# Optimization experiments

Measured on AMD Instinct MI355X. Metric: run time of the kernel, lower is better.

## Reference

```python
import jax, jax.numpy as jnp
import numpy as np

D_Q = 512
D_O = 256  # = d_v = d_k = d_o
N_HEAD = 8
BN_EPS = 1e-5
LEAK = 0.1


def setup_inputs() -> dict:
    key = jax.random.key(0)
    ks = jax.random.split(key, 8)
    s = 0.02
    inp = {
        "q": jax.random.normal(ks[0], (64, D_Q), dtype=jnp.float32),
        "v": jax.random.normal(ks[1], (64, D_O, 32, 32), dtype=jnp.float32),
        "w_q": jax.random.normal(ks[2], (D_O, D_Q), dtype=jnp.float32) * s,
        "b_q": jnp.zeros((D_O,), jnp.float32),
        "w_kc": jax.random.normal(ks[3], (D_O, D_O), dtype=jnp.float32) * s,
        "b_kc": jnp.zeros((D_O,), jnp.float32),
        "w_kd": jax.random.normal(ks[4], (D_O, D_O), dtype=jnp.float32) * s,
        "b_kd": jnp.zeros((D_O,), jnp.float32),
        "w_v": jax.random.normal(ks[5], (D_O, D_O), dtype=jnp.float32) * s,
        "b_v": jnp.zeros((D_O,), jnp.float32),
        "temp_c": jnp.asarray(1.0, jnp.float32),
        "temp_d": jnp.asarray(1.0, jnp.float32),
        "bn_gamma": jnp.ones((D_O,), jnp.float32),
        "bn_beta": jnp.zeros((D_O,), jnp.float32),
        "bn_mean": jnp.zeros((D_O,), jnp.float32),
        "bn_var": jnp.ones((D_O,), jnp.float32),
    }
    return inp


def _conv1x1(x, wgt, bias):
    # x: (b, c, h, w), wgt: (o, c) -> (b, o, h, w)
    return jnp.einsum('bchw,oc->bohw', x, wgt) + bias[None, :, None, None]


def reference(q, v, w_q, b_q, w_kc, b_kc, w_kd, b_kd, w_v, b_v,
              temp_c, temp_d, bn_gamma, bn_beta, bn_mean, bn_var):
    b = q.shape[0]
    _, c_v, h, w = v.shape
    n = N_HEAD
    dh = D_O // n
    hw = h * w
    residual = v

    # projections
    qv = (q @ w_q.T + b_q).reshape(b, n, dh)                      # (b, n, dh)
    kc = _conv1x1(v, w_kc, b_kc).reshape(b, n, dh, hw).transpose(0, 1, 3, 2)  # (b, n, hw, dh)
    kd = _conv1x1(v, w_kd, b_kd).reshape(b, n, dh, hw).transpose(0, 1, 3, 2)
    vp = _conv1x1(v, w_v, b_v).reshape(b, n, dh, hw).transpose(0, 1, 3, 2)

    # collect: softmax attention with query length 1
    col_logit = jnp.einsum('bnd,bnsd->bns', qv, kc) / temp_c      # (b, n, hw)
    attn_col = jax.nn.softmax(col_logit, axis=2)
    attn = jnp.einsum('bns,bnsd->bnd', attn_col, vp)              # (b, n, dh)

    # diffuse: sigmoid gate, outer product with collected vector
    dif = jax.nn.sigmoid(jnp.einsum('bnsd,bnd->bns', kd, qv) / temp_d)  # (b, n, hw)
    out = jnp.einsum('bns,bnd->bnsd', dif, attn)                  # (b, n, hw, dh)

    # faithful to torch permute(0,1,4,3,2).view: swaps h and w (requires h==w)
    out = out.reshape(b, n, h, w, dh).transpose(0, 1, 4, 3, 2).reshape(b, D_O, w, h)
    out = out + residual

    # BatchNorm2d (eval: running stats) + LeakyReLU(0.1); dropout is identity at eval
    inv = bn_gamma / jnp.sqrt(bn_var + BN_EPS)
    out = (out - bn_mean[None, :, None, None]) * inv[None, :, None, None] + bn_beta[None, :, None, None]
    out = jnp.where(out >= 0, out, LEAK * out)
    return out
```

## Files before the change

### kernel.cpp

```cpp
#include <hip/hip_runtime.h>
#include <math.h>

#define B    64
#define DQ   512
#define DO   256
#define NH   8
#define DH   32
#define HW   1024
#define NCH  16
#define CHS  64
#define CG   32
#define NT   (DO/CG)

__global__ __launch_bounds__(256) void k1_qv(const float* __restrict__ q,
                                             const float* __restrict__ w_q,
                                             const float* __restrict__ b_q,
                                             float* __restrict__ qv) {
    int cg = blockIdx.x, b = blockIdx.y;
    int t = threadIdx.x;
    int wid = t >> 6, lane = t & 63;
    const float4* qrow = reinterpret_cast<const float4*>(q + (size_t)b*DQ);
    float4 q0 = qrow[lane*2], q1 = qrow[lane*2 + 1];
    #pragma unroll
    for (int r = 0; r < 4; ++r) {
        int c = cg*16 + wid*4 + r;
        const float4* wrow = reinterpret_cast<const float4*>(w_q + (size_t)c*DQ);
        float4 w0 = wrow[lane*2], w1 = wrow[lane*2 + 1];
        float acc = q0.x*w0.x + q0.y*w0.y + q0.z*w0.z + q0.w*w0.w
                  + q1.x*w1.x + q1.y*w1.y + q1.z*w1.z + q1.w*w1.w;
        #pragma unroll
        for (int k = 32; k > 0; k >>= 1) acc += __shfl_xor(acc, k);
        if (lane == 0) qv[b*DO + c] = acc + b_q[c];
    }
}

__global__ void k2_wqk(const float* __restrict__ qv,
                       const float* __restrict__ w_kc, const float* __restrict__ b_kc,
                       const float* __restrict__ w_kd, const float* __restrict__ b_kd,
                       const float* __restrict__ temp_c, const float* __restrict__ temp_d,
                       float* __restrict__ wqkc, float* __restrict__ wqkd,
                       float* __restrict__ qbc, float* __restrict__ qbd) {
    int bn = blockIdx.x;
    int n  = bn & 7;
    int t  = threadIdx.x;
    __shared__ float qvs[DH];
    if (t < DH) qvs[t] = qv[(bn >> 3)*DO + n*DH + t];
    __syncthreads();
    float itc = 1.0f / temp_c[0];
    float itd = 1.0f / temp_d[0];
    float ac = 0.f, ad = 0.f;
    #pragma unroll
    for (int d = 0; d < DH; ++d) {
        float qd = qvs[d];
        ac += qd * w_kc[(n*DH + d)*DO + t];
        ad += qd * w_kd[(n*DH + d)*DO + t];
    }
    wqkc[bn*DO + t] = ac * itc;
    wqkd[bn*DO + t] = ad * itd;
    if (t == 0) {
        float sc = 0.f;
        for (int d = 0; d < DH; ++d) sc += qvs[d]*b_kc[n*DH + d];
        qbc[bn] = sc * itc;
    }
    if (t == 1) {
        float sd = 0.f;
        for (int d = 0; d < DH; ++d) sd += qvs[d]*b_kd[n*DH + d];
        qbd[bn] = sd * itd;
    }
}

__global__ __launch_bounds__(512, 8)
void k3i(const float* __restrict__ v,
         const float* __restrict__ wqkc, const float* __restrict__ wqkd,
         const float* __restrict__ qbc,  const float* __restrict__ qbd,
         float* __restrict__ gate, float* __restrict__ pvp, float* __restrict__ mz) {
    __shared__ float buf[2][CG][CHS];
    __shared__ float e_lds[NH][CHS];
    int ch = blockIdx.x, b = blockIdx.y;
    int t  = threadIdx.x;
    int s0 = ch*CHS;
    int bn0 = b*NH;
    int lane = t & 63;
    int w = __builtin_amdgcn_readfirstlane(t >> 6);

    int srow = t >> 4, sc4 = (t & 15)*4;
    const float* vb = v + (size_t)b*DO*HW + s0;

    {
        float4 st = *reinterpret_cast<const float4*>(vb + (size_t)srow*HW + sc4);
        *reinterpret_cast<float4*>(&buf[0][srow][sc4]) = st;
    }
    __syncthreads();

    float lc = qbc[bn0 + w];
    float ld = qbd[bn0 + w];
    const float* wcn = wqkc + (size_t)(bn0 + w)*DO;
    const float* wdn = wqkd + (size_t)(bn0 + w)*DO;
    #pragma unroll
    for (int g = 0; g < NT; ++g) {
        int cur = g & 1;
        float4 nx;
        if (g < NT-1)
            nx = *reinterpret_cast<const float4*>(vb + (size_t)((g+1)*CG + srow)*HW + sc4);
        int cbase = g*CG;
        #pragma unroll
        for (int cc = 0; cc < CG; ++cc) {
            float vv = buf[cur][cc][lane];
            lc = fmaf(wcn[cbase + cc], vv, lc);
            ld = fmaf(wdn[cbase + cc], vv, ld);
        }
        if (g < NT-1)
            *reinterpret_cast<float4*>(&buf[cur ^ 1][srow][sc4]) = nx;
        __syncthreads();
    }

    {
        gate[(size_t)(bn0 + w)*HW + s0 + lane] = 1.0f/(1.0f + __expf(-ld));
        float m = lc;
        #pragma unroll
        for (int k = 32; k > 0; k >>= 1) m = fmaxf(m, __shfl_xor(m, k));
        float e = __expf(lc - m);
        e_lds[w][lane] = e;
        float z = e;
        #pragma unroll
        for (int k = 32; k > 0; k >>= 1) z += __shfl_xor(z, k);
        if (lane == 0) {
            float* mzp = mz + ((size_t)(b*NCH + ch)*NH + w)*2;
            mzp[0] = m; mzp[1] = z;
        }
    }
    __syncthreads();

    {
        int ng = t >> 8;
        int c  = t & 255;
        const float* vrow = v + ((size_t)(b*DO + c))*HW + s0;
        float a0 = 0.f, a1 = 0.f, a2 = 0.f, a3 = 0.f;
        #pragma unroll
        for (int j = 0; j < CHS/4; ++j) {
            float4 v4 = *reinterpret_cast<const float4*>(vrow + j*4);
            float4 e0 = *reinterpret_cast<const float4*>(&e_lds[ng*4+0][j*4]);
            float4 e1 = *reinterpret_cast<const float4*>(&e_lds[ng*4+1][j*4]);
            float4 e2 = *reinterpret_cast<const float4*>(&e_lds[ng*4+2][j*4]);
            float4 e3 = *reinterpret_cast<const float4*>(&e_lds[ng*4+3][j*4]);
            a0 += v4.x*e0.x + v4.y*e0.y + v4.z*e0.z + v4.w*e0.w;
            a1 += v4.x*e1.x + v4.y*e1.y + v4.z*e1.z + v4.w*e1.w;
            a2 += v4.x*e2.x + v4.y*e2.y + v4.z*e2.z + v4.w*e2.w;
            a3 += v4.x*e3.x + v4.y*e3.y + v4.z*e3.z + v4.w*e3.w;
        }
        size_t pb = ((size_t)(b*NCH + ch)*NH + ng*4)*DO + c;
        pvp[pb]        = a0;
        pvp[pb + DO]   = a1;
        pvp[pb + 2*DO] = a2;
        pvp[pb + 3*DO] = a3;
    }
}

__global__ void k4c(const float* __restrict__ pvp, const float* __restrict__ mz,
                    const float* __restrict__ w_v, const float* __restrict__ b_v,
                    float* __restrict__ attn) {
    __shared__ float scale[NCH][NH];
    __shared__ float pv_lds[NH*DO];
    int b = blockIdx.x, t = threadIdx.x;
    if (t < NH) {
        int n = t;
        float M = -1e30f;
        for (int ch = 0; ch < NCH; ++ch)
            M = fmaxf(M, mz[((size_t)(b*NCH+ch)*NH+n)*2]);
        float Z = 0.f;
        for (int ch = 0; ch < NCH; ++ch) {
            float sc = __expf(mz[((size_t)(b*NCH+ch)*NH+n)*2] - M);
            Z += sc * mz[((size_t)(b*NCH+ch)*NH+n)*2 + 1];
            scale[ch][n] = sc;
        }
        float inv = 1.0f/Z;
        for (int ch = 0; ch < NCH; ++ch) scale[ch][n] *= inv;
    }
    __syncthreads();
    #pragma unroll
    for (int r = 0; r < 2; ++r) {
        int i4 = t + r*256;
        int n  = i4 >> 6;
        float4 s = make_float4(0.f, 0.f, 0.f, 0.f);
        #pragma unroll
        for (int ch = 0; ch < NCH; ++ch) {
            float sc = scale[ch][n];
            float4 p = reinterpret_cast<const float4*>(pvp + (size_t)(b*NCH + ch)*NH*DO)[i4];
            s.x = fmaf(sc, p.x, s.x); s.y = fmaf(sc, p.y, s.y);
            s.z = fmaf(sc, p.z, s.z); s.w = fmaf(sc, p.w, s.w);
        }
        *reinterpret_cast<float4*>(&pv_lds[i4*4]) = s;
    }
    __syncthreads();
    int n = t >> 5;
    float acc = b_v[t];
    const float4* w4 = reinterpret_cast<const float4*>(w_v + t*DO);
    #pragma unroll 4
    for (int c4 = 0; c4 < DO/4; ++c4) {
        float4 wv = w4[c4];
        int c = c4*4;
        acc += pv_lds[n*DO+c]*wv.x + pv_lds[n*DO+c+1]*wv.y + pv_lds[n*DO+c+2]*wv.z + pv_lds[n*DO+c+3]*wv.w;
    }
    attn[b*DO + t] = acc;
}

__global__ void k5_out(const float* __restrict__ v, const float* __restrict__ gate,
                       const float* __restrict__ attn,
                       const float* __restrict__ bn_g, const float* __restrict__ bn_b,
                       const float* __restrict__ bn_m, const float* __restrict__ bn_v,
                       float* __restrict__ out) {
    int c = blockIdx.x, b = blockIdx.y;
    int n = c >> 5, d = c & 31;
    int t = threadIdx.x;
    __shared__ float g[32*33];
    float4 gv = reinterpret_cast<const float4*>(gate + (b*NH + n)*HW)[t];
    int s0 = t*4;
    int ga = s0 >> 5, gb = s0 & 31;
    g[ga*33 + gb + 0] = gv.x;
    g[ga*33 + gb + 1] = gv.y;
    g[ga*33 + gb + 2] = gv.z;
    g[ga*33 + gb + 3] = gv.w;
    __syncthreads();
    float av   = attn[(b*NH + n)*DH + d];
    float inv  = bn_g[c] / sqrtf(bn_v[c] + 1e-5f);
    float mean = bn_m[c], beta = bn_b[c];
    size_t base = ((size_t)(b*DO + c))*HW;
    float4 r4 = reinterpret_cast<const float4*>(v + base)[t];
    int l = 4*t;
    int i_ = l >> 5, j_ = l & 31;
    float x0 = g[(j_+0)*33 + i_]*av + r4.x;
    float x1 = g[(j_+1)*33 + i_]*av + r4.y;
    float x2 = g[(j_+2)*33 + i_]*av + r4.z;
    float x3 = g[(j_+3)*33 + i_]*av + r4.w;
    float y0 = (x0 - mean)*inv + beta; y0 = y0 >= 0.f ? y0 : 0.1f*y0;
    float y1 = (x1 - mean)*inv + beta; y1 = y1 >= 0.f ? y1 : 0.1f*y1;
    float y2 = (x2 - mean)*inv + beta; y2 = y2 >= 0.f ? y2 : 0.1f*y2;
    float y3 = (x3 - mean)*inv + beta; y3 = y3 >= 0.f ? y3 : 0.1f*y3;
    reinterpret_cast<float4*>(out + base)[t] = make_float4(y0, y1, y2, y3);
}

extern "C" void kernel_launch(void* const* d_in, const int* in_sizes, int n_in,
                              void* d_out, int out_size, void* d_ws, size_t ws_size,
                              hipStream_t stream) {
    const float* q      = (const float*)d_in[0];
    const float* v      = (const float*)d_in[1];
    const float* w_q    = (const float*)d_in[2];
    const float* b_q    = (const float*)d_in[3];
    const float* w_kc   = (const float*)d_in[4];
    const float* b_kc   = (const float*)d_in[5];
    const float* w_kd   = (const float*)d_in[6];
    const float* b_kd   = (const float*)d_in[7];
    const float* w_v    = (const float*)d_in[8];
    const float* b_v    = (const float*)d_in[9];
    const float* temp_c = (const float*)d_in[10];
    const float* temp_d = (const float*)d_in[11];
    const float* bn_g   = (const float*)d_in[12];
    const float* bn_b   = (const float*)d_in[13];
    const float* bn_m   = (const float*)d_in[14];
    const float* bn_v   = (const float*)d_in[15];
    float* out = (float*)d_out;

    float* ws   = (float*)d_ws;
    float* qv   = ws;
    float* wqkc = qv   + B*DO;
    float* wqkd = wqkc + B*NH*DO;
    float* qbc  = wqkd + B*NH*DO;
    float* qbd  = qbc  + B*NH;
    float* gate = qbd  + B*NH;
    float* mz   = gate + B*NH*HW;
    float* pvp  = mz   + B*NCH*NH*2;
    float* attn = pvp  + B*NCH*NH*DO;

    k1_qv <<<dim3(16, B),    256, 0, stream>>>(q, w_q, b_q, qv);
    k2_wqk<<<B*NH,           256, 0, stream>>>(qv, w_kc, b_kc, w_kd, b_kd, temp_c, temp_d,
                                               wqkc, wqkd, qbc, qbd);
    k3i   <<<dim3(NCH, B),   512, 0, stream>>>(v, wqkc, wqkd, qbc, qbd, gate, pvp, mz);
    k4c   <<<B,              256, 0, stream>>>(pvp, mz, w_v, b_v, attn);
    k5_out<<<dim3(DO, B),    256, 0, stream>>>(v, gate, attn, bn_g, bn_b, bn_m, bn_v, out);
}
```

Measured before the change: 81.26 us.

## Stage full V chunk in swizzled LDS and reuse it for the PV partials

The main attention kernel now loads the whole 256x64 V chunk into a single XOR-swizzled shared buffer up front, instead of double-buffering 32-channel slices with a barrier per slice. The logit pass reads from this buffer with two independent accumulator pairs. The second-phase V·e reduction also reads V from LDS rather than re-reading it from global memory, with two threads per channel combined by a shuffle. This removes the second global read of V and most barriers, at the cost of 64KB of LDS per block, which lowers occupancy (launch bounds changed from 8 to 4).

```diff
diff --git a/kernel.cpp b/kernel.cpp
--- a/kernel.cpp
+++ b/kernel.cpp
@@ -9,8 +9,6 @@
 #define HW   1024
 #define NCH  16
 #define CHS  64
-#define CG   32
-#define NT   (DO/CG)
 
 __global__ __launch_bounds__(256) void k1_qv(const float* __restrict__ q,
                                              const float* __restrict__ w_q,
@@ -69,12 +67,12 @@
     }
 }
 
-__global__ __launch_bounds__(512, 8)
-void k3i(const float* __restrict__ v,
+__global__ __launch_bounds__(512, 4)
+void k3j(const float* __restrict__ v,
          const float* __restrict__ wqkc, const float* __restrict__ wqkd,
          const float* __restrict__ qbc,  const float* __restrict__ qbd,
          float* __restrict__ gate, float* __restrict__ pvp, float* __restrict__ mz) {
-    __shared__ float buf[2][CG][CHS];
+    __shared__ float vbuf[DO][CHS];
     __shared__ float e_lds[NH][CHS];
     int ch = blockIdx.x, b = blockIdx.y;
     int t  = threadIdx.x;
@@ -83,38 +81,48 @@
     int lane = t & 63;
     int w = __builtin_amdgcn_readfirstlane(t >> 6);
 
-    int srow = t >> 4, sc4 = (t & 15)*4;
-    const float* vb = v + (size_t)b*DO*HW + s0;
-
-    {
-        float4 st = *reinterpret_cast<const float4*>(vb + (size_t)srow*HW + sc4);
-        *reinterpret_cast<float4*>(&buf[0][srow][sc4]) = st;
-    }
-    __syncthreads();
-
-    float lc = qbc[bn0 + w];
-    float ld = qbd[bn0 + w];
-    const float* wcn = wqkc + (size_t)(bn0 + w)*DO;
-    const float* wdn = wqkd + (size_t)(bn0 + w)*DO;
-    #pragma unroll
-    for (int g = 0; g < NT; ++g) {
-        int cur = g & 1;
-        float4 nx;
-        if (g < NT-1)
-            nx = *reinterpret_cast<const float4*>(vb + (size_t)((g+1)*CG + srow)*HW + sc4);
-        int cbase = g*CG;
-        #pragma unroll
-        for (int cc = 0; cc < CG; ++cc) {
-            float vv = buf[cur][cc][lane];
-            lc = fmaf(wcn[cbase + cc], vv, lc);
-            ld = fmaf(wdn[cbase + cc], vv, ld);
-        }
-        if (g < NT-1)
-            *reinterpret_cast<float4*>(&buf[cur ^ 1][srow][sc4]) = nx;
-        __syncthreads();
-    }
-
-    {
+    {
+        int s4 = t & 15, srow = t >> 4;
+        const float* vb = v + (size_t)b*DO*HW + s0;
+        float4 r0 = *reinterpret_cast<const float4*>(vb + (size_t)(0*32+srow)*HW + s4*4);
+        float4 r1 = *reinterpret_cast<const float4*>(vb + (size_t)(1*32+srow)*HW + s4*4);
+        float4 r2 = *reinterpret_cast<const float4*>(vb + (size_t)(2*32+srow)*HW + s4*4);
+        float4 r3 = *reinterpret_cast<const float4*>(vb + (size_t)(3*32+srow)*HW + s4*4);
+        float4 r4 = *reinterpret_cast<const float4*>(vb + (size_t)(4*32+srow)*HW + s4*4);
+        float4 r5 = *reinterpret_cast<const float4*>(vb + (size_t)(5*32+srow)*HW + s4*4);
+        float4 r6 = *reinterpret_cast<const float4*>(vb + (size_t)(6*32+srow)*HW + s4*4);
+        float4 r7 = *reinterpret_cast<const float4*>(vb + (size_t)(7*32+srow)*HW + s4*4);
+        int idx4 = (s4 ^ (srow & 15)) * 4;
+        *reinterpret_cast<float4*>(&vbuf[0*32+srow][idx4]) = r0;
+        *reinterpret_cast<float4*>(&vbuf[1*32+srow][idx4]) = r1;
+        *reinterpret_cast<float4*>(&vbuf[2*32+srow][idx4]) = r2;
+        *reinterpret_cast<float4*>(&vbuf[3*32+srow][idx4]) = r3;
+        *reinterpret_cast<float4*>(&vbuf[4*32+srow][idx4]) = r4;
+        *reinterpret_cast<float4*>(&vbuf[5*32+srow][idx4]) = r5;
+        *reinterpret_cast<float4*>(&vbuf[6*32+srow][idx4]) = r6;
+        *reinterpret_cast<float4*>(&vbuf[7*32+srow][idx4]) = r7;
+    }
+    __syncthreads();
+
+    float lcA = 0.f, lcB = 0.f, ldA = 0.f, ldB = 0.f;
+    {
+        const float* wcn = wqkc + (size_t)(bn0 + w)*DO;
+        const float* wdn = wqkd + (size_t)(bn0 + w)*DO;
+        int sq = lane >> 2, sk = lane & 3;
+        #pragma unroll 8
+        for (int c = 0; c < DO; c += 2) {
+            float v0 = vbuf[c    ][((sq ^ (c     & 15)) << 2) | sk];
+            float v1 = vbuf[c + 1][((sq ^ ((c+1) & 15)) << 2) | sk];
+            lcA = fmaf(wcn[c],   v0, lcA);
+            ldA = fmaf(wdn[c],   v0, ldA);
+            lcB = fmaf(wcn[c+1], v1, lcB);
+            ldB = fmaf(wdn[c+1], v1, ldB);
+        }
+    }
+
+    {
+        float lc = lcA + lcB + qbc[bn0 + w];
+        float ld = ldA + ldB + qbd[bn0 + w];
         gate[(size_t)(bn0 + w)*HW + s0 + lane] = 1.0f/(1.0f + __expf(-ld));
         float m = lc;
         #pragma unroll
@@ -132,27 +140,32 @@
     __syncthreads();
 
     {
-        int ng = t >> 8;
-        int c  = t & 255;
-        const float* vrow = v + ((size_t)(b*DO + c))*HW + s0;
-        float a0 = 0.f, a1 = 0.f, a2 = 0.f, a3 = 0.f;
-        #pragma unroll
-        for (int j = 0; j < CHS/4; ++j) {
-            float4 v4 = *reinterpret_cast<const float4*>(vrow + j*4);
-            float4 e0 = *reinterpret_cast<const float4*>(&e_lds[ng*4+0][j*4]);
-            float4 e1 = *reinterpret_cast<const float4*>(&e_lds[ng*4+1][j*4]);
-            float4 e2 = *reinterpret_cast<const float4*>(&e_lds[ng*4+2][j*4]);
-            float4 e3 = *reinterpret_cast<const float4*>(&e_lds[ng*4+3][j*4]);
-            a0 += v4.x*e0.x + v4.y*e0.y + v4.z*e0.z + v4.w*e0.w;
-            a1 += v4.x*e1.x + v4.y*e1.y + v4.z*e1.z + v4.w*e1.w;
-            a2 += v4.x*e2.x + v4.y*e2.y + v4.z*e2.z + v4.w*e2.w;
-            a3 += v4.x*e3.x + v4.y*e3.y + v4.z*e3.z + v4.w*e3.w;
-        }
-        size_t pb = ((size_t)(b*NCH + ch)*NH + ng*4)*DO + c;
-        pvp[pb]        = a0;
-        pvp[pb + DO]   = a1;
-        pvp[pb + 2*DO] = a2;
-        pvp[pb + 3*DO] = a3;
+        int c = t >> 1, sh = t & 1;
+        int cx = (c & 15);
+        float4 vr[8];
+        #pragma unroll
+        for (int j = 0; j < 8; ++j) {
+            int s4r = sh*8 + j;
+            vr[j] = *reinterpret_cast<const float4*>(&vbuf[c][(s4r ^ cx) * 4]);
+        }
+        float acc[NH];
+        #pragma unroll
+        for (int n = 0; n < NH; ++n) {
+            float a = 0.f;
+            #pragma unroll
+            for (int j = 0; j < 8; ++j) {
+                int s4r = sh*8 + j;
+                float4 e4 = *reinterpret_cast<const float4*>(&e_lds[n][s4r*4]);
+                a += vr[j].x*e4.x + vr[j].y*e4.y + vr[j].z*e4.z + vr[j].w*e4.w;
+            }
+            a += __shfl_xor(a, 1);
+            acc[n] = a;
+        }
+        if (sh == 0) {
+            size_t pb = ((size_t)(b*NCH + ch)*NH)*DO + c;
+            #pragma unroll
+            for (int n = 0; n < NH; ++n) pvp[pb + n*DO] = acc[n];
+        }
     }
 }
 
@@ -182,7 +195,7 @@
         int i4 = t + r*256;
         int n  = i4 >> 6;
         float4 s = make_float4(0.f, 0.f, 0.f, 0.f);
-        #pragma unroll
+        #pragma unroll 4
         for (int ch = 0; ch < NCH; ++ch) {
             float sc = scale[ch][n];
             float4 p = reinterpret_cast<const float4*>(pvp + (size_t)(b*NCH + ch)*NH*DO)[i4];
@@ -274,7 +287,7 @@
     k1_qv <<<dim3(16, B),    256, 0, stream>>>(q, w_q, b_q, qv);
     k2_wqk<<<B*NH,           256, 0, stream>>>(qv, w_kc, b_kc, w_kd, b_kd, temp_c, temp_d,
                                                wqkc, wqkd, qbc, qbd);
-    k3i   <<<dim3(NCH, B),   512, 0, stream>>>(v, wqkc, wqkd, qbc, qbd, gate, pvp, mz);
+    k3j   <<<dim3(NCH, B),   512, 0, stream>>>(v, wqkc, wqkd, qbc, qbd, gate, pvp, mz);
     k4c   <<<B,              256, 0, stream>>>(pvp, mz, w_v, b_v, attn);
     k5_out<<<dim3(DO, B),    256, 0, stream>>>(v, gate, attn, bn_g, bn_b, bn_m, bn_v, out);
 }
```

New measurement: 80.30 us. Within noise of the previous version (-1.2%).

## Register-tile v chunk in k3 and reuse it for logits and pooled values

Applied to the files above, without the earlier changes.

The logit kernel now loads each thread's slice of the v chunk into registers once. It computes all 8 heads' collect and diffuse logits as register-tiled outer products against transposed per-batch weight vectors staged in LDS, then reduces partial sums across lanes and waves. The same registers are reused for the softmax-weighted pooling, which removes the second global read of v and the double-buffered LDS staging loop. The cost is higher register pressure (launch bounds lowered to 4 blocks), many cross-lane shuffles, and a convoluted select-based output write.

```diff
diff --git a/kernel.cpp b/kernel.cpp
--- a/kernel.cpp
+++ b/kernel.cpp
@@ -9,8 +9,6 @@
 #define HW   1024
 #define NCH  16
 #define CHS  64
-#define CG   32
-#define NT   (DO/CG)
 
 __global__ __launch_bounds__(256) void k1_qv(const float* __restrict__ q,
                                              const float* __restrict__ w_q,
@@ -38,13 +36,14 @@
                        const float* __restrict__ w_kc, const float* __restrict__ b_kc,
                        const float* __restrict__ w_kd, const float* __restrict__ b_kd,
                        const float* __restrict__ temp_c, const float* __restrict__ temp_d,
-                       float* __restrict__ wqkc, float* __restrict__ wqkd,
+                       float* __restrict__ wqkcT, float* __restrict__ wqkdT,
                        float* __restrict__ qbc, float* __restrict__ qbd) {
     int bn = blockIdx.x;
     int n  = bn & 7;
+    int bb = bn >> 3;
     int t  = threadIdx.x;
     __shared__ float qvs[DH];
-    if (t < DH) qvs[t] = qv[(bn >> 3)*DO + n*DH + t];
+    if (t < DH) qvs[t] = qv[bb*DO + n*DH + t];
     __syncthreads();
     float itc = 1.0f / temp_c[0];
     float itd = 1.0f / temp_d[0];
@@ -55,8 +54,8 @@
         ac += qd * w_kc[(n*DH + d)*DO + t];
         ad += qd * w_kd[(n*DH + d)*DO + t];
     }
-    wqkc[bn*DO + t] = ac * itc;
-    wqkd[bn*DO + t] = ad * itd;
+    wqkcT[((size_t)bb*DO + t)*NH + n] = ac * itc;
+    wqkdT[((size_t)bb*DO + t)*NH + n] = ad * itd;
     if (t == 0) {
         float sc = 0.f;
         for (int d = 0; d < DH; ++d) sc += qvs[d]*b_kc[n*DH + d];
@@ -69,12 +68,13 @@
     }
 }
 
-__global__ __launch_bounds__(512, 8)
-void k3i(const float* __restrict__ v,
-         const float* __restrict__ wqkc, const float* __restrict__ wqkd,
+__global__ __launch_bounds__(512, 4)
+void k3k(const float* __restrict__ v,
+         const float* __restrict__ wqkcT, const float* __restrict__ wqkdT,
          const float* __restrict__ qbc,  const float* __restrict__ qbd,
          float* __restrict__ gate, float* __restrict__ pvp, float* __restrict__ mz) {
-    __shared__ float buf[2][CG][CHS];
+    __shared__ float wt[2][DO][NH];
+    __shared__ float pex[2][NH][NH][CHS];
     __shared__ float e_lds[NH][CHS];
     int ch = blockIdx.x, b = blockIdx.y;
     int t  = threadIdx.x;
@@ -82,39 +82,80 @@
     int bn0 = b*NH;
     int lane = t & 63;
     int w = __builtin_amdgcn_readfirstlane(t >> 6);
-
-    int srow = t >> 4, sc4 = (t & 15)*4;
-    const float* vb = v + (size_t)b*DO*HW + s0;
+    int c4 = lane >> 4, s4 = lane & 15;
+    int cbase = w*32;
 
     {
-        float4 st = *reinterpret_cast<const float4*>(vb + (size_t)srow*HW + sc4);
-        *reinterpret_cast<float4*>(&buf[0][srow][sc4]) = st;
-    }
-    __syncthreads();
-
-    float lc = qbc[bn0 + w];
-    float ld = qbd[bn0 + w];
-    const float* wcn = wqkc + (size_t)(bn0 + w)*DO;
-    const float* wdn = wqkd + (size_t)(bn0 + w)*DO;
+        const float4* sc_ = reinterpret_cast<const float4*>(wqkcT + (size_t)b*DO*NH);
+        const float4* sd_ = reinterpret_cast<const float4*>(wqkdT + (size_t)b*DO*NH);
+        reinterpret_cast<float4*>(&wt[0][0][0])[t] = sc_[t];
+        reinterpret_cast<float4*>(&wt[1][0][0])[t] = sd_[t];
+    }
+
+    float4 vreg[8];
+    {
+        const float* vb = v + (size_t)b*DO*HW + s0;
+        #pragma unroll
+        for (int ci = 0; ci < 8; ++ci) {
+            int c = cbase + ci*4 + c4;
+            vreg[ci] = *reinterpret_cast<const float4*>(vb + (size_t)c*HW + s4*4);
+        }
+    }
+    __syncthreads();
+
     #pragma unroll
-    for (int g = 0; g < NT; ++g) {
-        int cur = g & 1;
-        float4 nx;
-        if (g < NT-1)
-            nx = *reinterpret_cast<const float4*>(vb + (size_t)((g+1)*CG + srow)*HW + sc4);
-        int cbase = g*CG;
-        #pragma unroll
-        for (int cc = 0; cc < CG; ++cc) {
-            float vv = buf[cur][cc][lane];
-            lc = fmaf(wcn[cbase + cc], vv, lc);
-            ld = fmaf(wdn[cbase + cc], vv, ld);
-        }
-        if (g < NT-1)
-            *reinterpret_cast<float4*>(&buf[cur ^ 1][srow][sc4]) = nx;
-        __syncthreads();
-    }
+    for (int hp = 0; hp < 2; ++hp) {
+        float acc_c[4][4] = {{0,0,0,0},{0,0,0,0},{0,0,0,0},{0,0,0,0}};
+        float acc_d[4][4] = {{0,0,0,0},{0,0,0,0},{0,0,0,0},{0,0,0,0}};
+        #pragma unroll
+        for (int ci = 0; ci < 8; ++ci) {
+            int c = cbase + ci*4 + c4;
+            float4 wc4 = *reinterpret_cast<const float4*>(&wt[0][c][hp*4]);
+            float4 wd4 = *reinterpret_cast<const float4*>(&wt[1][c][hp*4]);
+            float4 vv = vreg[ci];
+            float wcv[4] = {wc4.x, wc4.y, wc4.z, wc4.w};
+            float wdv[4] = {wd4.x, wd4.y, wd4.z, wd4.w};
+            #pragma unroll
+            for (int n = 0; n < 4; ++n) {
+                float a = wcv[n], d = wdv[n];
+                acc_c[n][0] = fmaf(a, vv.x, acc_c[n][0]);
+                acc_c[n][1] = fmaf(a, vv.y, acc_c[n][1]);
+                acc_c[n][2] = fmaf(a, vv.z, acc_c[n][2]);
+                acc_c[n][3] = fmaf(a, vv.w, acc_c[n][3]);
+                acc_d[n][0] = fmaf(d, vv.x, acc_d[n][0]);
+                acc_d[n][1] = fmaf(d, vv.y, acc_d[n][1]);
+                acc_d[n][2] = fmaf(d, vv.z, acc_d[n][2]);
+                acc_d[n][3] = fmaf(d, vv.w, acc_d[n][3]);
+            }
+        }
+        #pragma unroll
+        for (int n = 0; n < 4; ++n)
+            #pragma unroll
+            for (int j = 0; j < 4; ++j) {
+                acc_c[n][j] += __shfl_xor(acc_c[n][j], 16);
+                acc_c[n][j] += __shfl_xor(acc_c[n][j], 32);
+                acc_d[n][j] += __shfl_xor(acc_d[n][j], 16);
+                acc_d[n][j] += __shfl_xor(acc_d[n][j], 32);
+            }
+        if (c4 == 0) {
+            #pragma unroll
+            for (int n = 0; n < 4; ++n) {
+                *reinterpret_cast<float4*>(&pex[0][w][hp*4+n][s4*4])
+                    = make_float4(acc_c[n][0], acc_c[n][1], acc_c[n][2], acc_c[n][3]);
+                *reinterpret_cast<float4*>(&pex[1][w][hp*4+n][s4*4])
+                    = make_float4(acc_d[n][0], acc_d[n][1], acc_d[n][2], acc_d[n][3]);
+            }
+        }
+    }
+    __syncthreads();
 
     {
+        float lc = qbc[bn0 + w], ld = qbd[bn0 + w];
+        #pragma unroll
+        for (int k = 0; k < 8; ++k) {
+            lc += pex[0][k][w][lane];
+            ld += pex[1][k][w][lane];
+        }
         gate[(size_t)(bn0 + w)*HW + s0 + lane] = 1.0f/(1.0f + __expf(-ld));
         float m = lc;
         #pragma unroll
@@ -132,27 +173,46 @@
     __syncthreads();
 
     {
-        int ng = t >> 8;
-        int c  = t & 255;
-        const float* vrow = v + ((size_t)(b*DO + c))*HW + s0;
-        float a0 = 0.f, a1 = 0.f, a2 = 0.f, a3 = 0.f;
-        #pragma unroll
-        for (int j = 0; j < CHS/4; ++j) {
-            float4 v4 = *reinterpret_cast<const float4*>(vrow + j*4);
-            float4 e0 = *reinterpret_cast<const float4*>(&e_lds[ng*4+0][j*4]);
-            float4 e1 = *reinterpret_cast<const float4*>(&e_lds[ng*4+1][j*4]);
-            float4 e2 = *reinterpret_cast<const float4*>(&e_lds[ng*4+2][j*4]);
-            float4 e3 = *reinterpret_cast<const float4*>(&e_lds[ng*4+3][j*4]);
-            a0 += v4.x*e0.x + v4.y*e0.y + v4.z*e0.z + v4.w*e0.w;
-            a1 += v4.x*e1.x + v4.y*e1.y + v4.z*e1.z + v4.w*e1.w;
-            a2 += v4.x*e2.x + v4.y*e2.y + v4.z*e2.z + v4.w*e2.w;
-            a3 += v4.x*e3.x + v4.y*e3.y + v4.z*e3.z + v4.w*e3.w;
-        }
-        size_t pb = ((size_t)(b*NCH + ch)*NH + ng*4)*DO + c;
-        pvp[pb]        = a0;
-        pvp[pb + DO]   = a1;
-        pvp[pb + 2*DO] = a2;
-        pvp[pb + 3*DO] = a3;
+        float pool[8][8];
+        #pragma unroll
+        for (int n = 0; n < 8; ++n) {
+            float4 e4 = *reinterpret_cast<const float4*>(&e_lds[n][s4*4]);
+            #pragma unroll
+            for (int ci = 0; ci < 8; ++ci) {
+                float4 vv = vreg[ci];
+                pool[n][ci] = vv.x*e4.x + vv.y*e4.y + vv.z*e4.z + vv.w*e4.w;
+            }
+        }
+        #pragma unroll
+        for (int n = 0; n < 8; ++n)
+            #pragma unroll
+            for (int ci = 0; ci < 8; ++ci) {
+                pool[n][ci] += __shfl_xor(pool[n][ci], 1);
+                pool[n][ci] += __shfl_xor(pool[n][ci], 2);
+                pool[n][ci] += __shfl_xor(pool[n][ci], 4);
+                pool[n][ci] += __shfl_xor(pool[n][ci], 8);
+            }
+        size_t pb = ((size_t)(b*NCH + ch)*NH)*DO;
+        int wn = s4 >> 1;
+        int ci0 = (s4 & 1)*4;
+        float o0, o1, o2, o3;
+        #pragma unroll
+        for (int n = 0; n < 8; ++n) {
+            #pragma unroll
+            for (int ci = 0; ci < 8; ++ci) {
+                if (n == 0 && ci == 0) { o0 = pool[0][0]; o1 = pool[0][4]; o2 = pool[0][1]; o3 = pool[0][5]; }
+            }
+        }
+        #pragma unroll
+        for (int k = 0; k < 4; ++k) {
+            float val = 0.f;
+            #pragma unroll
+            for (int n = 0; n < 8; ++n)
+                #pragma unroll
+                for (int cj = 0; cj < 8; ++cj)
+                    val = (n == wn && cj == ci0 + k) ? pool[n][cj] : val;
+            pvp[pb + (size_t)wn*DO + cbase + (ci0 + k)*4 + c4] = val;
+        }
     }
 }
 
@@ -182,7 +242,7 @@
         int i4 = t + r*256;
         int n  = i4 >> 6;
         float4 s = make_float4(0.f, 0.f, 0.f, 0.f);
-        #pragma unroll
+        #pragma unroll 4
         for (int ch = 0; ch < NCH; ++ch) {
             float sc = scale[ch][n];
             float4 p = reinterpret_cast<const float4*>(pvp + (size_t)(b*NCH + ch)*NH*DO)[i4];
@@ -260,21 +320,21 @@
     const float* bn_v   = (const float*)d_in[15];
     float* out = (float*)d_out;
 
-    float* ws   = (float*)d_ws;
-    float* qv   = ws;
-    float* wqkc = qv   + B*DO;
-    float* wqkd = wqkc + B*NH*DO;
-    float* qbc  = wqkd + B*NH*DO;
-    float* qbd  = qbc  + B*NH;
-    float* gate = qbd  + B*NH;
-    float* mz   = gate + B*NH*HW;
-    float* pvp  = mz   + B*NCH*NH*2;
-    float* attn = pvp  + B*NCH*NH*DO;
+    float* ws    = (float*)d_ws;
+    float* qv    = ws;
+    float* wqkcT = qv    + B*DO;
+    float* wqkdT = wqkcT + B*DO*NH;
+    float* qbc   = wqkdT + B*DO*NH;
+    float* qbd   = qbc   + B*NH;
+    float* gate  = qbd   + B*NH;
+    float* mz    = gate  + B*NH*HW;
+    float* pvp   = mz    + B*NCH*NH*2;
+    float* attn  = pvp   + (size_t)B*NCH*NH*DO;
 
     k1_qv <<<dim3(16, B),    256, 0, stream>>>(q, w_q, b_q, qv);
     k2_wqk<<<B*NH,           256, 0, stream>>>(qv, w_kc, b_kc, w_kd, b_kd, temp_c, temp_d,
-                                               wqkc, wqkd, qbc, qbd);
-    k3i   <<<dim3(NCH, B),   512, 0, stream>>>(v, wqkc, wqkd, qbc, qbd, gate, pvp, mz);
+                                               wqkcT, wqkdT, qbc, qbd);
+    k3k   <<<dim3(NCH, B),   512, 0, stream>>>(v, wqkcT, wqkdT, qbc, qbd, gate, pvp, mz);
     k4c   <<<B,              256, 0, stream>>>(pvp, mz, w_v, b_v, attn);
     k5_out<<<dim3(DO, B),    256, 0, stream>>>(v, gate, attn, bn_g, bn_b, bn_m, bn_v, out);
 }
```

After: 95.79 us. 17.9% more time.
